# Kernel tuning notes

Hardware: AMD Instinct MI355X
Metric: run time of the kernel (lower is better)

The kernel has to match this reference:

```python
import jax, jax.numpy as jnp
import numpy as np

# ---- static config (matches init_kwargs) ----
DIM = 96
H = W = D = 28
WS = 7            # window size
SS = 3            # shift size
NH = 4            # num heads
HD = DIM // NH    # head dim
SCALE = HD ** -0.5
NWIN_TOK = WS ** 3  # 343 tokens per window
HIDDEN = int(DIM * 4.0)
RPB_SIZE = (2 * WS - 1) ** 3


def _relative_position_index(ws):
    # faithful to source: rel[...,0] *= 2*ws-1 ; rel[...,1] *= 2*ws-1
    coords = np.stack(np.meshgrid(np.arange(ws), np.arange(ws), np.arange(ws), indexing='ij'))
    flat = coords.reshape(3, -1)                      # (3, N)
    rel = flat[:, :, None] - flat[:, None, :]         # (3, N, N)
    rel = rel.transpose(1, 2, 0).astype(np.int64)     # (N, N, 3)
    rel += ws - 1
    rel[:, :, 0] *= 2 * ws - 1
    rel[:, :, 1] *= 2 * ws - 1
    return rel.sum(-1)                                # (N, N)


def _attn_mask(Hh, Ww, Dd, ws, ss):
    img = np.zeros((1, Hh, Ww, Dd, 1), np.float32)
    cnt = 0
    sl = (slice(0, -ws), slice(-ws, -ss), slice(-ss, None))
    for a in sl:
        for b in sl:
            for c in sl:
                img[:, a, b, c, :] = cnt
                cnt += 1
    x = img.reshape(1, Hh // ws, ws, Ww // ws, ws, Dd // ws, ws, 1)
    mw = x.transpose(0, 1, 3, 5, 2, 4, 6, 7).reshape(-1, ws ** 3)  # (nW, N)
    am = mw[:, None, :] - mw[:, :, None]                           # (nW, N, N)
    return np.where(am != 0, -100.0, 0.0).astype(np.float32)


RPI = jnp.asarray(_relative_position_index(WS))          # (N, N) int
ATTN_MASK = jnp.asarray(_attn_mask(H, W, D, WS, SS))     # (nW, N, N)


def _ln(x, w, b, eps=1e-5):
    mu = x.mean(-1, keepdims=True)
    xc = x - mu
    var = (xc * xc).mean(-1, keepdims=True)
    return xc * jax.lax.rsqrt(var + eps) * w + b


def _window_partition(x):
    # x: (B, H, W, D, C) -> (B*nW, N, C)
    B, _, _, _, C = x.shape
    x = x.reshape(B, H // WS, WS, W // WS, WS, D // WS, WS, C)
    return x.transpose(0, 1, 3, 5, 2, 4, 6, 7).reshape(-1, NWIN_TOK, C)


def _window_reverse(wins, B):
    C = wins.shape[-1]
    x = wins.reshape(B, H // WS, W // WS, D // WS, WS, WS, WS, C)
    return x.transpose(0, 1, 4, 2, 5, 3, 6, 7).reshape(B, H, W, D, C)


def setup_inputs() -> dict:
    key = jax.random.key(0)
    ks = jax.random.split(key, 16)
    p = lambda k, shape, s: (jax.random.normal(k, shape, jnp.float32) * s)
    return {
        'x': jax.random.normal(ks[0], (4, H * W * D, DIM), jnp.float32),
        'norm1_w': jnp.ones((DIM,), jnp.float32),
        'norm1_b': jnp.zeros((DIM,), jnp.float32),
        'qkv_w': p(ks[1], (DIM, 3 * DIM), 0.02),   # (in, out)
        'qkv_b': jnp.zeros((3 * DIM,), jnp.float32),
        'rpb_table': p(ks[2], (RPB_SIZE, NH), 0.02),
        'proj_w': p(ks[3], (DIM, DIM), 0.02),
        'proj_b': jnp.zeros((DIM,), jnp.float32),
        'norm2_w': jnp.ones((DIM,), jnp.float32),
        'norm2_b': jnp.zeros((DIM,), jnp.float32),
        'fc1_w': p(ks[4], (DIM, HIDDEN), 0.02),
        'fc1_b': jnp.zeros((HIDDEN,), jnp.float32),
        'fc2_w': p(ks[5], (HIDDEN, DIM), 0.02),
        'fc2_b': jnp.zeros((DIM,), jnp.float32),
    }


def reference(x, norm1_w, norm1_b, qkv_w, qkv_b, rpb_table, proj_w, proj_b,
              norm2_w, norm2_b, fc1_w, fc1_b, fc2_w, fc2_b):
    B, L, C = x.shape
    shortcut = x

    xn = _ln(x, norm1_w, norm1_b).reshape(B, H, W, D, C)
    # cyclic shift (SW-MSA)
    xs = jnp.roll(xn, (-SS, -SS, -SS), axis=(1, 2, 3))
    xw = _window_partition(xs)                        # (B_, N, C)
    B_ = xw.shape[0]
    Nn = NWIN_TOK

    qkv = (xw @ qkv_w + qkv_b).reshape(B_, Nn, 3, NH, HD).transpose(2, 0, 3, 1, 4)
    q, k, v = qkv[0], qkv[1], qkv[2]                  # (B_, h, N, hd)
    attn = jnp.einsum('bhnd,bhmd->bhnm', q * SCALE, k)

    # relative position bias gather: (N*N,) -> (N, N, h) -> (h, N, N)
    rpb = rpb_table[RPI.reshape(-1)].reshape(Nn, Nn, NH).transpose(2, 0, 1)
    attn = attn + rpb[None]

    nW = ATTN_MASK.shape[0]
    attn = attn.reshape(B, nW, NH, Nn, Nn) + ATTN_MASK[None, :, None]
    attn = jax.nn.softmax(attn.reshape(B_, NH, Nn, Nn), axis=-1)

    out = jnp.einsum('bhnm,bhmd->bhnd', attn, v).transpose(0, 2, 1, 3).reshape(B_, Nn, C)
    out = out @ proj_w + proj_b

    xr = _window_reverse(out, B)
    xr = jnp.roll(xr, (SS, SS, SS), axis=(1, 2, 3)).reshape(B, L, C)

    x = shortcut + xr                                  # drop_path = 0 (eval)
    y = _ln(x, norm2_w, norm2_b)
    y = jax.nn.gelu(y @ fc1_w + fc1_b, approximate=False)
    return x + (y @ fc2_w + fc2_b)
```

## Files before the change

### kernel.cpp

```cpp
#include <hip/hip_runtime.h>

#define NTOK 343
#define NP   352
#define SCALE 0.2041241452319315f
#define VSTR 360
#define PSTR 40

typedef __attribute__((ext_vector_type(8))) short bf16x8;
typedef __attribute__((ext_vector_type(4))) float f32x4;

__device__ __forceinline__ unsigned short f2bf(float f){
  unsigned u = __builtin_bit_cast(unsigned, f);
  u += 0x7fffu + ((u >> 16) & 1u);
  return (unsigned short)(u >> 16);
}
__device__ __forceinline__ float bfel(const uint4& q, int t){
  unsigned u = (&q.x)[t >> 1];
  u = (t & 1) ? (u & 0xffff0000u) : (u << 16);
  return __builtin_bit_cast(float, u);
}
__device__ __forceinline__ unsigned pk2(float a, float b){
  unsigned ua = __builtin_bit_cast(unsigned, a) + 0x8000u;
  unsigned ub = __builtin_bit_cast(unsigned, b) + 0x8000u;
  return __builtin_amdgcn_perm(ub, ua, 0x07060302u);
}
__device__ __forceinline__ unsigned pkrn(float a, float b){
  return (unsigned)f2bf(a) | ((unsigned)f2bf(b) << 16);
}
__device__ __forceinline__ int region(int g){ return (g < 21) ? 0 : ((g < 25) ? 1 : 2); }

__global__ __launch_bounds__(256) void k_rpb(const float* __restrict__ tab, float* __restrict__ rpbB){
  const int bid = blockIdx.x, tid = threadIdx.x;
  const int lane = tid >> 2, reg = tid & 3;
  const int qt = bid % 22, tmp = bid / 22, kt = tmp % 22, hh = tmp / 22;
  const int n = lane & 15, qd = lane >> 4;
  const int i = qt * 16 + n;
  const int j = kt * 16 + qd * 4 + reg;
  float v;
  if (j >= NTOK) v = -1e30f;
  else if (i >= NTOK) v = 0.f;
  else {
    int r1 = i / 49, rm = i - r1 * 49, r2 = rm / 7, r3 = rm - r2 * 7;
    int j1 = j / 49, jm = j - j1 * 49, j2 = jm / 7, j3 = jm - j2 * 7;
    int idx = 13 * ((r1 - j1) + (r2 - j2) + 12) + (r3 - j3) + 6;
    v = tab[idx * 4 + hh];
  }
  rpbB[(size_t)bid * 256 + tid] = v;
}

__global__ __launch_bounds__(256) void k_wprep1(const float* __restrict__ qw, unsigned short* __restrict__ wQ){
  int p = blockIdx.x * 256 + threadIdx.x;
  int e = p & 7, m = (p >> 3) & 15, cell = p >> 7;
  int mt = cell / 12, kq = cell - mt * 12;
  wQ[p] = f2bf(qw[(kq * 8 + e) * 288 + mt * 16 + m]);
}

__global__ __launch_bounds__(256) void k_wprep2(
    const float* __restrict__ pw, const float* __restrict__ w1g, const float* __restrict__ w2g,
    unsigned short* __restrict__ w1F, unsigned short* __restrict__ w2F, unsigned short* __restrict__ wP)
{
  int p = blockIdx.x * 256 + threadIdx.x;
  if (p < 36864){
    int e = p & 7, m = (p >> 3) & 15, cell = p >> 7;
    int mt = cell / 12, q = cell - mt * 12;
    w1F[p] = f2bf(w1g[(q * 8 + e) * 384 + mt * 16 + m]);
  } else if (p < 73728){
    int p2 = p - 36864;
    int e = p2 & 7, m = (p2 >> 3) & 15, cell = p2 >> 7;
    int omt = cell / 48, q = cell - omt * 48;
    w2F[p2] = f2bf(w2g[(q * 8 + e) * 96 + omt * 16 + m]);
  } else {
    int p3 = p - 73728;
    int e = p3 & 7, m = (p3 >> 3) & 15, cell = p3 >> 7;
    int mt = cell / 12, kq = cell - mt * 12;
    wP[p3] = f2bf(pw[(kq * 8 + e) * 96 + mt * 16 + m]);
  }
}

__global__ __launch_bounds__(256, 4) void k_qkv(
    const float* __restrict__ x, const float* __restrict__ n1w, const float* __restrict__ n1b,
    const unsigned short* __restrict__ wQ, const float* __restrict__ qb,
    unsigned short* __restrict__ qS, unsigned short* __restrict__ kS, unsigned short* __restrict__ vS)
{
  __shared__ __align__(16) unsigned short xnF[11 * 12 * 16 * 8];
  const int blk = blockIdx.x, w = blk >> 1, half = blk & 1;
  const int b = w >> 6, wl = w & 63;
  const int wx = wl >> 4, wy = (wl >> 2) & 3, wz = wl & 3;
  const int tid = threadIdx.x, lane = tid & 63, wv = tid >> 6;

  const float g1 = n1w[lane], h1 = n1b[lane];
  const float g2 = (lane < 32) ? n1w[64 + lane] : 0.f;
  const float h2 = (lane < 32) ? n1b[64 + lane] : 0.f;
  for (int r = wv; r < 176; r += 4){
    int tl = half * 176 + r;
    int tok = (tl < NTOK) ? tl : NTOK - 1;
    int tx = tok / 49, rm = tok - tx * 49, ty = rm / 7, tz = rm - ty * 7;
    int sx = (wx * 7 + tx + 3) % 28, sy = (wy * 7 + ty + 3) % 28, sz = (wz * 7 + tz + 3) % 28;
    const float* xr = x + ((size_t)b * 21952 + ((sx * 28 + sy) * 28 + sz)) * 96;
    float v1 = xr[lane];
    float v2 = (lane < 32) ? xr[64 + lane] : 0.f;
    float s = v1 + v2, sq = v1 * v1 + v2 * v2;
    #pragma unroll
    for (int off = 32; off; off >>= 1){ s += __shfl_xor(s, off); sq += __shfl_xor(sq, off); }
    float mu = s * (1.f / 96.f);
    float rs = rsqrtf(sq * (1.f / 96.f) - mu * mu + 1e-5f);
    int nt = r >> 4, n = r & 15;
    xnF[((nt * 12 + (lane >> 3)) * 16 + n) * 8 + (lane & 7)] = f2bf((v1 - mu) * rs * g1 + h1);
    if (lane < 32){
      int cc = 64 + lane;
      xnF[((nt * 12 + (cc >> 3)) * 16 + n) * 8 + (cc & 7)] = f2bf((v2 - mu) * rs * g2 + h2);
    }
  }
  __syncthreads();

  const int ln = lane & 15, qd = lane >> 4;
  bf16x8 bfr[3][3];
  int nts[3], toks[3];
  #pragma unroll
  for (int t = 0; t < 3; t++){
    int nt = wv + 4 * t;
    nts[t] = (nt < 11) ? nt : -1;
    int ntc = (nt < 11) ? nt : 0;
    toks[t] = half * 176 + ntc * 16 + ln;
    #pragma unroll
    for (int ks = 0; ks < 3; ks++)
      bfr[t][ks] = *(const bf16x8*)(xnF + ((ntc * 12 + ks * 4 + qd) * 16 + ln) * 8);
  }
  for (int mt = 0; mt < 18; mt++){
    bf16x8 afr[3];
    #pragma unroll
    for (int ks = 0; ks < 3; ks++)
      afr[ks] = *(const bf16x8*)(wQ + ((mt * 12 + ks * 4 + qd) * 16 + ln) * 8);
    f32x4 acc[3];
    #pragma unroll
    for (int t = 0; t < 3; t++){ acc[t][0] = 0.f; acc[t][1] = 0.f; acc[t][2] = 0.f; acc[t][3] = 0.f; }
    #pragma unroll
    for (int ks = 0; ks < 3; ks++)
      #pragma unroll
      for (int t = 0; t < 3; t++)
        acc[t] = __builtin_amdgcn_mfma_f32_16x16x32_bf16(afr[ks], bfr[t][ks], acc[t], 0, 0, 0);
    const int o0 = mt * 16 + 4 * qd;
    float4 bv = *(const float4*)(qb + o0);
    const int s3 = o0 / 96, om = o0 - s3 * 96, hh = om / 24, d = om - hh * 24;
    const float sc = (s3 == 0) ? SCALE : 1.f;
    unsigned short* base = (s3 == 0) ? qS : ((s3 == 1) ? kS : vS);
    unsigned short* hb = base + ((size_t)(w * 4 + hh)) * 8232 + d;
    #pragma unroll
    for (int t = 0; t < 3; t++){
      if (nts[t] < 0) continue;
      if (toks[t] < NTOK){
        uint2 st;
        st.x = pkrn((acc[t][0] + bv.x) * sc, (acc[t][1] + bv.y) * sc);
        st.y = pkrn((acc[t][2] + bv.z) * sc, (acc[t][3] + bv.w) * sc);
        *(uint2*)(hb + (size_t)toks[t] * 24) = st;
      }
    }
  }
}

__global__ __launch_bounds__(256, 2) void k_attn(
    const unsigned short* __restrict__ qS, const unsigned short* __restrict__ kS,
    const unsigned short* __restrict__ vS, const float* __restrict__ rpbB,
    unsigned short* __restrict__ aO)
{
  __shared__ __align__(16) unsigned short Ksh[NP * 24];
  __shared__ __align__(16) unsigned short VTsh[24 * VSTR];
  __shared__ __align__(16) unsigned short Psh[4 * 16 * PSTR];
  __shared__ __align__(8) unsigned char lab8[NP];

  const int blk = blockIdx.x, w = blk >> 2, h = blk & 3;
  const int tid = threadIdx.x, lane = tid & 63, wv = tid >> 6;
  const int ln = lane & 15, qd = lane >> 4;

  {
    const unsigned* kg = (const unsigned*)(kS + (size_t)blk * 8232);
    unsigned* kd = (unsigned*)Ksh;
    for (int i = tid; i < 4224; i += 256) kd[i] = (i < 4116) ? kg[i] : 0u;
    const unsigned* vg = (const unsigned*)(vS + (size_t)blk * 8232);
    for (int i = tid; i < 4116; i += 256){
      unsigned v = vg[i];
      int e0 = 2 * i, key = e0 / 24, d = e0 - key * 24;
      VTsh[d * VSTR + key] = (unsigned short)(v & 0xffffu);
      VTsh[(d + 1) * VSTR + key] = (unsigned short)(v >> 16);
    }
    for (int i = tid; i < 24 * 13; i += 256){
      int d = i / 13, kk = 343 + (i - d * 13);
      VTsh[d * VSTR + kk] = 0;
    }
    const int wl = w & 63, wx = wl >> 4, wy = (wl >> 2) & 3, wz = wl & 3;
    for (int n = tid; n < NP; n += 256){
      int tx = n / 49, nm = n - tx * 49, ty = nm / 7, tz = nm - ty * 7;
      lab8[n] = (n < NTOK) ? (unsigned char)(region(wx*7+tx)*9 + region(wy*7+ty)*3 + region(wz*7+tz)) : (unsigned char)0;
    }
  }
  __syncthreads();

  bf16x8 qf[6];
  int labQ[6], qts[6];
  #pragma unroll
  for (int t = 0; t < 6; t++){
    int qtr = wv + 4 * t;
    bool val = qtr < 22;
    qts[t] = val ? qtr : -1;
    int qt = val ? qtr : 0;
    int query = qt * 16 + ln;
    uint4 qv = *(const uint4*)(qS + (size_t)blk * 8232 + (size_t)query * 24 + qd * 8);
    if (qd == 3){ qv.x = 0; qv.y = 0; qv.z = 0; qv.w = 0; }
    qf[t] = __builtin_bit_cast(bf16x8, qv);
    labQ[t] = lab8[qt * 16 + ln];
  }

  f32x4 accO[6][2];
  float ssum[6];
  #pragma unroll
  for (int t = 0; t < 6; t++){
    ssum[t] = 0.f;
    #pragma unroll
    for (int d2 = 0; d2 < 2; d2++){ accO[t][d2][0]=0.f; accO[t][d2][1]=0.f; accO[t][d2][2]=0.f; accO[t][d2][3]=0.f; }
  }
  const float* biasBase = rpbB + (size_t)h * (22 * 22 * 256);
  unsigned short* pb = Psh + wv * 16 * PSTR + ln * PSTR;
  const unsigned short* pr = Psh + wv * 16 * PSTR + ln * PSTR + qd * 8;
  const int vt1row = 16 + (ln & 7);
  const f32x4 zf = {0.f, 0.f, 0.f, 0.f};

  for (int kp = 0; kp < 11; kp++){
    uint4 kv0 = *(const uint4*)(Ksh + (kp * 32 + ln) * 24 + qd * 8);
    uint4 kv1 = *(const uint4*)(Ksh + (kp * 32 + 16 + ln) * 24 + qd * 8);
    bf16x8 kf0 = __builtin_bit_cast(bf16x8, kv0);
    bf16x8 kf1 = __builtin_bit_cast(bf16x8, kv1);
    bf16x8 vf0 = *(const bf16x8*)(VTsh + ln * VSTR + kp * 32 + qd * 8);
    bf16x8 vf1 = *(const bf16x8*)(VTsh + vt1row * VSTR + kp * 32 + qd * 8);
    const unsigned* l32 = (const unsigned*)lab8;
    unsigned la = l32[kp * 8 + qd];
    unsigned lb = l32[kp * 8 + 4 + qd];
    int kl0[4], kl1[4];
    #pragma unroll
    for (int r = 0; r < 4; r++){ kl0[r] = (la >> (8 * r)) & 255; kl1[r] = (lb >> (8 * r)) & 255; }

    #pragma unroll
    for (int t = 0; t < 6; t++){
      if (qts[t] < 0) continue;
      const int qt = qts[t];
      f32x4 s0 = __builtin_amdgcn_mfma_f32_16x16x32_bf16(kf0, qf[t], zf, 0, 0, 0);
      f32x4 s1 = __builtin_amdgcn_mfma_f32_16x16x32_bf16(kf1, qf[t], zf, 0, 0, 0);
      const float* bp = biasBase + (((size_t)(2 * kp) * 22 + qt) * 64 + lane) * 4;
      float4 b0 = *(const float4*)bp;
      float4 b1 = *(const float4*)(bp + 22 * 256);
      const int lq = labQ[t];
      float e0[4], e1[4];
      #pragma unroll
      for (int r = 0; r < 4; r++){
        float ev = __expf(s0[r] + (&b0.x)[r]);
        e0[r] = (kl0[r] == lq) ? ev : 0.f;
      }
      #pragma unroll
      for (int r = 0; r < 4; r++){
        float ev = __expf(s1[r] + (&b1.x)[r]);
        e1[r] = (kl1[r] == lq) ? ev : 0.f;
      }
      ssum[t] += ((e0[0] + e0[1]) + (e0[2] + e0[3])) + ((e1[0] + e1[1]) + (e1[2] + e1[3]));
      uint2 w0; w0.x = pk2(e0[0], e0[1]); w0.y = pk2(e0[2], e0[3]);
      uint2 w1; w1.x = pk2(e1[0], e1[1]); w1.y = pk2(e1[2], e1[3]);
      *(uint2*)(pb + 4 * qd)      = w0;
      *(uint2*)(pb + 16 + 4 * qd) = w1;
      bf16x8 pf = *(const bf16x8*)pr;
      accO[t][0] = __builtin_amdgcn_mfma_f32_16x16x32_bf16(vf0, pf, accO[t][0], 0, 0, 0);
      accO[t][1] = __builtin_amdgcn_mfma_f32_16x16x32_bf16(vf1, pf, accO[t][1], 0, 0, 0);
    }
  }

  #pragma unroll
  for (int t = 0; t < 6; t++){
    if (qts[t] < 0) continue;
    float s = ssum[t];
    s += __shfl_xor(s, 16);
    s += __shfl_xor(s, 32);
    float inv = 1.f / s;
    int query = qts[t] * 16 + ln;
    if (query < NTOK){
      unsigned short* dst = aO + (size_t)w * 32928 + (size_t)query * 96 + h * 24;
      uint2 o0;
      o0.x = pkrn(accO[t][0][0] * inv, accO[t][0][1] * inv);
      o0.y = pkrn(accO[t][0][2] * inv, accO[t][0][3] * inv);
      *(uint2*)(dst + 4 * qd) = o0;
      if (qd < 2){
        uint2 o1;
        o1.x = pkrn(accO[t][1][0] * inv, accO[t][1][1] * inv);
        o1.y = pkrn(accO[t][1][2] * inv, accO[t][1][3] * inv);
        *(uint2*)(dst + 16 + 4 * qd) = o1;
      }
    }
  }
}

__global__ __launch_bounds__(256, 4) void k_proj(
    const unsigned short* __restrict__ aO, const unsigned short* __restrict__ wP,
    const float* __restrict__ pb, const float* __restrict__ x, float* __restrict__ out)
{
  __shared__ __align__(16) unsigned short aF[11 * 12 * 16 * 8];
  const int blk = blockIdx.x, w = blk >> 1, half = blk & 1;
  const int b = w >> 6, wl = w & 63;
  const int wx = wl >> 4, wy = (wl >> 2) & 3, wz = wl & 3;
  const int tid = threadIdx.x, lane = tid & 63, wv = tid >> 6;

  for (int i = tid; i < 2112; i += 256){
    int r = i / 12, kq = i - r * 12;
    int tl = half * 176 + r;
    uint4 v;
    if (tl < NTOK) v = *(const uint4*)(aO + (size_t)w * 32928 + (size_t)tl * 96 + kq * 8);
    else { v.x = 0u; v.y = 0u; v.z = 0u; v.w = 0u; }
    int nt = r >> 4, n = r & 15;
    *(uint4*)(aF + ((nt * 12 + kq) * 16 + n) * 8) = v;
  }
  __syncthreads();

  const int ln = lane & 15, qd = lane >> 4;
  bf16x8 bfr[3][3];
  int nts[3]; size_t oi[3]; bool tv[3];
  #pragma unroll
  for (int t = 0; t < 3; t++){
    int nt = wv + 4 * t;
    nts[t] = (nt < 11) ? nt : -1;
    int ntc = (nt < 11) ? nt : 0;
    int tok = half * 176 + ntc * 16 + ln;
    tv[t] = (nts[t] >= 0) && (tok < NTOK);
    int tk = (tok < NTOK) ? tok : 0;
    int tx = tk / 49, rm = tk - tx * 49, ty = rm / 7, tz = rm - ty * 7;
    int sx = (wx * 7 + tx + 3) % 28, sy = (wy * 7 + ty + 3) % 28, sz = (wz * 7 + tz + 3) % 28;
    oi[t] = ((size_t)b * 21952 + ((sx * 28 + sy) * 28 + sz)) * 96;
    #pragma unroll
    for (int ks = 0; ks < 3; ks++)
      bfr[t][ks] = *(const bf16x8*)(aF + ((ntc * 12 + ks * 4 + qd) * 16 + ln) * 8);
  }
  for (int mt = 0; mt < 6; mt++){
    bf16x8 afr[3];
    #pragma unroll
    for (int ks = 0; ks < 3; ks++)
      afr[ks] = *(const bf16x8*)(wP + ((mt * 12 + ks * 4 + qd) * 16 + ln) * 8);
    f32x4 acc[3];
    #pragma unroll
    for (int t = 0; t < 3; t++){ acc[t][0] = 0.f; acc[t][1] = 0.f; acc[t][2] = 0.f; acc[t][3] = 0.f; }
    #pragma unroll
    for (int ks = 0; ks < 3; ks++)
      #pragma unroll
      for (int t = 0; t < 3; t++)
        acc[t] = __builtin_amdgcn_mfma_f32_16x16x32_bf16(afr[ks], bfr[t][ks], acc[t], 0, 0, 0);
    const int c0 = mt * 16 + 4 * qd;
    float4 bv = *(const float4*)(pb + c0);
    #pragma unroll
    for (int t = 0; t < 3; t++){
      if (!tv[t]) continue;
      float4 cur = *(const float4*)(x + oi[t] + c0);
      float4 o;
      o.x = acc[t][0] + bv.x + cur.x;
      o.y = acc[t][1] + bv.y + cur.y;
      o.z = acc[t][2] + bv.z + cur.z;
      o.w = acc[t][3] + bv.w + cur.w;
      *(float4*)(out + oi[t] + c0) = o;
    }
  }
}

__global__ __launch_bounds__(256, 4) void k_mlp(
    float* __restrict__ io, const float* __restrict__ n2w, const float* __restrict__ n2b,
    const unsigned short* __restrict__ w1F, const float* __restrict__ b1g,
    const unsigned short* __restrict__ w2F, const float* __restrict__ b2g)
{
  __shared__ __align__(16) unsigned short xnF[2 * 12 * 16 * 8];
  __shared__ __align__(16) unsigned short hF[2 * 48 * 16 * 8];
  const int tid = threadIdx.x, lane = tid & 63, wv = tid >> 6;
  const size_t row0 = (size_t)blockIdx.x * 32;

  const float g1 = n2w[lane], c1 = n2b[lane];
  const float g2 = (lane < 32) ? n2w[64 + lane] : 0.f;
  const float c2 = (lane < 32) ? n2b[64 + lane] : 0.f;
  for (int r = wv; r < 32; r += 4){
    const float* xr = io + (row0 + r) * 96;
    float v1 = xr[lane], v2 = (lane < 32) ? xr[64 + lane] : 0.f;
    float s = v1 + v2, sq = v1 * v1 + v2 * v2;
    #pragma unroll
    for (int off = 32; off; off >>= 1){ s += __shfl_xor(s, off); sq += __shfl_xor(sq, off); }
    float mu = s * (1.f / 96.f);
    float rs = rsqrtf(sq * (1.f / 96.f) - mu * mu + 1e-5f);
    int nt = r >> 4, n = r & 15;
    xnF[((nt * 12 + (lane >> 3)) * 16 + n) * 8 + (lane & 7)] = f2bf((v1 - mu) * rs * g1 + c1);
    if (lane < 32){
      int cc = 64 + lane;
      xnF[((nt * 12 + (cc >> 3)) * 16 + n) * 8 + (cc & 7)] = f2bf((v2 - mu) * rs * g2 + c2);
    }
  }
  __syncthreads();

  const int h = lane & 15, q = lane >> 4;
  const int nt = wv & 1, mh = wv >> 1;

  f32x4 acc[12];
  #pragma unroll
  for (int mt = 0; mt < 12; mt++){
    int o0 = (mh * 12 + mt) * 16 + 4 * q;
    float4 bv = *(const float4*)(b1g + o0);
    acc[mt][0] = bv.x; acc[mt][1] = bv.y; acc[mt][2] = bv.z; acc[mt][3] = bv.w;
  }
  for (int ks = 0; ks < 3; ks++){
    bf16x8 bfr = *(const bf16x8*)(xnF + ((nt * 12 + ks * 4 + q) * 16 + h) * 8);
    #pragma unroll
    for (int mt = 0; mt < 12; mt++){
      bf16x8 afr = *(const bf16x8*)(w1F + (((mh * 12 + mt) * 12 + ks * 4 + q) * 16 + h) * 8);
      acc[mt] = __builtin_amdgcn_mfma_f32_16x16x32_bf16(afr, bfr, acc[mt], 0, 0, 0);
    }
  }
  #pragma unroll
  for (int mt = 0; mt < 12; mt++){
    int o0 = (mh * 12 + mt) * 16 + 4 * q;
    unsigned short pk[4];
    #pragma unroll
    for (int rg = 0; rg < 4; rg++){
      float v = acc[mt][rg];
      pk[rg] = f2bf(0.5f * v * (1.f + erff(v * 0.70710678118654752f)));
    }
    unsigned short* d = hF + ((nt * 48 + (o0 >> 3)) * 16 + h) * 8 + (o0 & 7);
    uint2 pkv; pkv.x = (unsigned)pk[0] | ((unsigned)pk[1] << 16);
    pkv.y = (unsigned)pk[2] | ((unsigned)pk[3] << 16);
    *(uint2*)d = pkv;
  }
  __syncthreads();

  f32x4 acc2[3];
  #pragma unroll
  for (int mt = 0; mt < 3; mt++){
    int o0 = (mh * 3 + mt) * 16 + 4 * q;
    float4 bv = *(const float4*)(b2g + o0);
    acc2[mt][0] = bv.x; acc2[mt][1] = bv.y; acc2[mt][2] = bv.z; acc2[mt][3] = bv.w;
  }
  for (int ks = 0; ks < 12; ks++){
    bf16x8 bfr = *(const bf16x8*)(hF + ((nt * 48 + ks * 4 + q) * 16 + h) * 8);
    #pragma unroll
    for (int mt = 0; mt < 3; mt++){
      bf16x8 afr = *(const bf16x8*)(w2F + (((mh * 3 + mt) * 48 + ks * 4 + q) * 16 + h) * 8);
      acc2[mt] = __builtin_amdgcn_mfma_f32_16x16x32_bf16(afr, bfr, acc2[mt], 0, 0, 0);
    }
  }
  float* orow = io + (row0 + nt * 16 + h) * 96;
  #pragma unroll
  for (int mt = 0; mt < 3; mt++){
    int o0 = (mh * 3 + mt) * 16 + 4 * q;
    float4 cur = *(const float4*)(orow + o0);
    cur.x += acc2[mt][0]; cur.y += acc2[mt][1]; cur.z += acc2[mt][2]; cur.w += acc2[mt][3];
    *(float4*)(orow + o0) = cur;
  }
}

extern "C" void kernel_launch(void* const* d_in, const int* in_sizes, int n_in,
                              void* d_out, int out_size, void* d_ws, size_t ws_size,
                              hipStream_t stream)
{
  const float* x      = (const float*)d_in[0];
  const float* n1w    = (const float*)d_in[1];
  const float* n1b    = (const float*)d_in[2];
  const float* qkvw   = (const float*)d_in[3];
  const float* qkvb   = (const float*)d_in[4];
  const float* rpbtab = (const float*)d_in[5];
  const float* projw  = (const float*)d_in[6];
  const float* projb  = (const float*)d_in[7];
  const float* n2w    = (const float*)d_in[8];
  const float* n2b    = (const float*)d_in[9];
  const float* fc1w   = (const float*)d_in[10];
  const float* fc1b   = (const float*)d_in[11];
  const float* fc2w   = (const float*)d_in[12];
  const float* fc2b   = (const float*)d_in[13];
  float* out = (float*)d_out;

  unsigned short* qS = (unsigned short*)d_ws;
  unsigned short* kS = qS + 8429568;
  unsigned short* vS = kS + 8429568;
  unsigned short* aO = vS + 8429568;
  float* rpbB = (float*)(aO + 8429568);
  unsigned short* wQ  = aO;
  unsigned short* w1F = qS;
  unsigned short* w2F = qS + 36864;
  unsigned short* wP  = qS + 73728;

  k_rpb   <<<dim3(1936), dim3(256), 0, stream>>>(rpbtab, rpbB);
  k_wprep1<<<dim3(108),  dim3(256), 0, stream>>>(qkvw, wQ);
  k_qkv   <<<dim3(512),  dim3(256), 0, stream>>>(x, n1w, n1b, wQ, qkvb, qS, kS, vS);
  k_attn  <<<dim3(1024), dim3(256), 0, stream>>>(qS, kS, vS, rpbB, aO);
  k_wprep2<<<dim3(324),  dim3(256), 0, stream>>>(projw, fc1w, fc2w, w1F, w2F, wP);
  k_proj  <<<dim3(512),  dim3(256), 0, stream>>>(aO, wP, projb, x, out);
  k_mlp   <<<dim3(2744), dim3(256), 0, stream>>>(out, n2w, n2b, w1F, fc1b, w2F, fc2b);
}
```

Baseline: 318.9 us.

## Restructure window attention: bf16 bias in MFMA accumulator, exp2, pre-transposed V, ones-row rowsum

The relative-position bias is stored as bf16 pre-scaled by log2(e) and loaded as the MFMA accumulator init, and Q is scaled by log2(e), so softmax uses exp2 with no separate bias add. k_qkv now writes V already transposed, which removes the shared-memory transpose in k_attn. K is read straight from global memory instead of staged in LDS. An extra all-ones row in V^T makes the PV MFMA produce the softmax row sum, dropping the scalar sum. Less LDS lets launch bounds rise to 4 blocks per SM, but bias precision drops to bf16 and the transposed V stores in k_qkv are scattered 2-byte writes.

Result: faster. 285.2 us (-10.6%).

```diff
diff --git a/kernel.cpp b/kernel.cpp
--- a/kernel.cpp
+++ b/kernel.cpp
@@ -3,6 +3,7 @@
 #define NTOK 343
 #define NP   352
 #define SCALE 0.2041241452319315f
+#define LOG2E 1.44269504088896340736f
 #define VSTR 360
 #define PSTR 40
 
@@ -14,11 +15,8 @@
   u += 0x7fffu + ((u >> 16) & 1u);
   return (unsigned short)(u >> 16);
 }
-__device__ __forceinline__ float bfel(const uint4& q, int t){
-  unsigned u = (&q.x)[t >> 1];
-  u = (t & 1) ? (u & 0xffff0000u) : (u << 16);
-  return __builtin_bit_cast(float, u);
-}
+__device__ __forceinline__ float bflo(unsigned u){ return __builtin_bit_cast(float, u << 16); }
+__device__ __forceinline__ float bfhi(unsigned u){ return __builtin_bit_cast(float, u & 0xffff0000u); }
 __device__ __forceinline__ unsigned pk2(float a, float b){
   unsigned ua = __builtin_bit_cast(unsigned, a) + 0x8000u;
   unsigned ub = __builtin_bit_cast(unsigned, b) + 0x8000u;
@@ -29,23 +27,26 @@
 }
 __device__ __forceinline__ int region(int g){ return (g < 21) ? 0 : ((g < 25) ? 1 : 2); }
 
-__global__ __launch_bounds__(256) void k_rpb(const float* __restrict__ tab, float* __restrict__ rpbB){
-  const int bid = blockIdx.x, tid = threadIdx.x;
-  const int lane = tid >> 2, reg = tid & 3;
-  const int qt = bid % 22, tmp = bid / 22, kt = tmp % 22, hh = tmp / 22;
-  const int n = lane & 15, qd = lane >> 4;
-  const int i = qt * 16 + n;
-  const int j = kt * 16 + qd * 4 + reg;
-  float v;
-  if (j >= NTOK) v = -1e30f;
-  else if (i >= NTOK) v = 0.f;
-  else {
-    int r1 = i / 49, rm = i - r1 * 49, r2 = rm / 7, r3 = rm - r2 * 7;
-    int j1 = j / 49, jm = j - j1 * 49, j2 = jm / 7, j3 = jm - j2 * 7;
-    int idx = 13 * ((r1 - j1) + (r2 - j2) + 12) + (r3 - j3) + 6;
-    v = tab[idx * 4 + hh];
-  }
-  rpbB[(size_t)bid * 256 + tid] = v;
+__global__ __launch_bounds__(256) void k_rpb(const float* __restrict__ tab, unsigned short* __restrict__ rpbH){
+  const int bid = blockIdx.x;
+  const int qt = bid % 22, t2 = bid / 22, kp = t2 % 11, h = t2 / 11;
+  for (int e = threadIdx.x; e < 512; e += 256){
+    int lane = e >> 3, slot = e & 7;
+    int kth = slot >> 2, reg = slot & 3;
+    int n = lane & 15, qd = lane >> 4;
+    int i = qt * 16 + n;
+    int j = (2 * kp + kth) * 16 + qd * 4 + reg;
+    float v;
+    if (j >= NTOK) v = -1e30f;
+    else if (i >= NTOK) v = 0.f;
+    else {
+      int r1 = i / 49, rm = i - r1 * 49, r2 = rm / 7, r3 = rm - r2 * 7;
+      int j1 = j / 49, jm = j - j1 * 49, j2 = jm / 7, j3 = jm - j2 * 7;
+      int idx = 13 * ((r1 - j1) + (r2 - j2) + 12) + (r3 - j3) + 6;
+      v = tab[idx * 4 + h] * LOG2E;
+    }
+    rpbH[(size_t)bid * 512 + e] = f2bf(v);
+  }
 }
 
 __global__ __launch_bounds__(256) void k_wprep1(const float* __restrict__ qw, unsigned short* __restrict__ wQ){
@@ -80,7 +81,7 @@
 __global__ __launch_bounds__(256, 4) void k_qkv(
     const float* __restrict__ x, const float* __restrict__ n1w, const float* __restrict__ n1b,
     const unsigned short* __restrict__ wQ, const float* __restrict__ qb,
-    unsigned short* __restrict__ qS, unsigned short* __restrict__ kS, unsigned short* __restrict__ vS)
+    unsigned short* __restrict__ qS, unsigned short* __restrict__ kS, unsigned short* __restrict__ vT)
 {
   __shared__ __align__(16) unsigned short xnF[11 * 12 * 16 * 8];
   const int blk = blockIdx.x, w = blk >> 1, half = blk & 1;
@@ -141,30 +142,38 @@
         acc[t] = __builtin_amdgcn_mfma_f32_16x16x32_bf16(afr[ks], bfr[t][ks], acc[t], 0, 0, 0);
     const int o0 = mt * 16 + 4 * qd;
     float4 bv = *(const float4*)(qb + o0);
-    const int s3 = o0 / 96, om = o0 - s3 * 96, hh = om / 24, d = om - hh * 24;
-    const float sc = (s3 == 0) ? SCALE : 1.f;
-    unsigned short* base = (s3 == 0) ? qS : ((s3 == 1) ? kS : vS);
-    unsigned short* hb = base + ((size_t)(w * 4 + hh)) * 8232 + d;
-    #pragma unroll
-    for (int t = 0; t < 3; t++){
-      if (nts[t] < 0) continue;
-      if (toks[t] < NTOK){
+    const int s3 = o0 / 96, om = o0 - s3 * 96, hh = om / 24, dd = om - hh * 24;
+    if (s3 < 2){
+      const float sc = (s3 == 0) ? (SCALE * LOG2E) : 1.f;
+      unsigned short* hb = ((s3 == 0) ? qS : kS) + ((size_t)(w * 4 + hh)) * 8232 + dd;
+      #pragma unroll
+      for (int t = 0; t < 3; t++){
+        if (nts[t] < 0 || toks[t] >= NTOK) continue;
         uint2 st;
         st.x = pkrn((acc[t][0] + bv.x) * sc, (acc[t][1] + bv.y) * sc);
         st.y = pkrn((acc[t][2] + bv.z) * sc, (acc[t][3] + bv.w) * sc);
         *(uint2*)(hb + (size_t)toks[t] * 24) = st;
       }
-    }
-  }
-}
-
-__global__ __launch_bounds__(256, 2) void k_attn(
+    } else {
+      unsigned short* hb = vT + ((size_t)(w * 4 + hh)) * 8256 + (size_t)dd * 344;
+      #pragma unroll
+      for (int t = 0; t < 3; t++){
+        if (nts[t] < 0 || toks[t] >= NTOK) continue;
+        hb[0 * 344 + toks[t]] = f2bf(acc[t][0] + bv.x);
+        hb[1 * 344 + toks[t]] = f2bf(acc[t][1] + bv.y);
+        hb[2 * 344 + toks[t]] = f2bf(acc[t][2] + bv.z);
+        hb[3 * 344 + toks[t]] = f2bf(acc[t][3] + bv.w);
+      }
+    }
+  }
+}
+
+__global__ __launch_bounds__(256, 4) void k_attn(
     const unsigned short* __restrict__ qS, const unsigned short* __restrict__ kS,
-    const unsigned short* __restrict__ vS, const float* __restrict__ rpbB,
+    const unsigned short* __restrict__ vT, const unsigned short* __restrict__ rpbH,
     unsigned short* __restrict__ aO)
 {
-  __shared__ __align__(16) unsigned short Ksh[NP * 24];
-  __shared__ __align__(16) unsigned short VTsh[24 * VSTR];
+  __shared__ __align__(16) unsigned short VTsh[25 * VSTR];
   __shared__ __align__(16) unsigned short Psh[4 * 16 * PSTR];
   __shared__ __align__(8) unsigned char lab8[NP];
 
@@ -173,20 +182,17 @@
   const int ln = lane & 15, qd = lane >> 4;
 
   {
-    const unsigned* kg = (const unsigned*)(kS + (size_t)blk * 8232);
-    unsigned* kd = (unsigned*)Ksh;
-    for (int i = tid; i < 4224; i += 256) kd[i] = (i < 4116) ? kg[i] : 0u;
-    const unsigned* vg = (const unsigned*)(vS + (size_t)blk * 8232);
-    for (int i = tid; i < 4116; i += 256){
-      unsigned v = vg[i];
-      int e0 = 2 * i, key = e0 / 24, d = e0 - key * 24;
-      VTsh[d * VSTR + key] = (unsigned short)(v & 0xffffu);
-      VTsh[(d + 1) * VSTR + key] = (unsigned short)(v >> 16);
-    }
-    for (int i = tid; i < 24 * 13; i += 256){
-      int d = i / 13, kk = 343 + (i - d * 13);
-      VTsh[d * VSTR + kk] = 0;
-    }
+    const unsigned* vg = (const unsigned*)(vT + (size_t)blk * 8256);
+    unsigned* vd = (unsigned*)VTsh;
+    for (int i = tid; i < 4128; i += 256){
+      int d = i / 172, c = i - d * 172;
+      vd[d * 180 + c] = vg[i];
+    }
+    for (int i = tid; i < 192; i += 256){
+      int d = i >> 3, c = i & 7;
+      vd[d * 180 + 172 + c] = 0u;
+    }
+    for (int i = tid; i < 180; i += 256) vd[24 * 180 + i] = 0x3f803f80u;
     const int wl = w & 63, wx = wl >> 4, wy = (wl >> 2) & 3, wz = wl & 3;
     for (int n = tid; n < NP; n += 256){
       int tx = n / 49, nm = n - tx * 49, ty = nm / 7, tz = nm - ty * 7;
@@ -211,26 +217,24 @@
   }
 
   f32x4 accO[6][2];
-  float ssum[6];
-  #pragma unroll
-  for (int t = 0; t < 6; t++){
-    ssum[t] = 0.f;
+  #pragma unroll
+  for (int t = 0; t < 6; t++)
     #pragma unroll
     for (int d2 = 0; d2 < 2; d2++){ accO[t][d2][0]=0.f; accO[t][d2][1]=0.f; accO[t][d2][2]=0.f; accO[t][d2][3]=0.f; }
-  }
-  const float* biasBase = rpbB + (size_t)h * (22 * 22 * 256);
+
+  const unsigned short* biasBase = rpbH + (size_t)h * (11 * 22 * 512);
   unsigned short* pb = Psh + wv * 16 * PSTR + ln * PSTR;
   const unsigned short* pr = Psh + wv * 16 * PSTR + ln * PSTR + qd * 8;
-  const int vt1row = 16 + (ln & 7);
-  const f32x4 zf = {0.f, 0.f, 0.f, 0.f};
+  const int vrow1 = (ln < 8) ? (16 + ln) : 24;
+  const size_t kbase = (size_t)blk * 8232;
 
   for (int kp = 0; kp < 11; kp++){
-    uint4 kv0 = *(const uint4*)(Ksh + (kp * 32 + ln) * 24 + qd * 8);
-    uint4 kv1 = *(const uint4*)(Ksh + (kp * 32 + 16 + ln) * 24 + qd * 8);
+    uint4 kv0 = *(const uint4*)(kS + kbase + (size_t)(kp * 32 + ln) * 24 + qd * 8);
+    uint4 kv1 = *(const uint4*)(kS + kbase + (size_t)(kp * 32 + 16 + ln) * 24 + qd * 8);
     bf16x8 kf0 = __builtin_bit_cast(bf16x8, kv0);
     bf16x8 kf1 = __builtin_bit_cast(bf16x8, kv1);
     bf16x8 vf0 = *(const bf16x8*)(VTsh + ln * VSTR + kp * 32 + qd * 8);
-    bf16x8 vf1 = *(const bf16x8*)(VTsh + vt1row * VSTR + kp * 32 + qd * 8);
+    bf16x8 vf1 = *(const bf16x8*)(VTsh + vrow1 * VSTR + kp * 32 + qd * 8);
     const unsigned* l32 = (const unsigned*)lab8;
     unsigned la = l32[kp * 8 + qd];
     unsigned lb = l32[kp * 8 + 4 + qd];
@@ -242,24 +246,24 @@
     for (int t = 0; t < 6; t++){
       if (qts[t] < 0) continue;
       const int qt = qts[t];
-      f32x4 s0 = __builtin_amdgcn_mfma_f32_16x16x32_bf16(kf0, qf[t], zf, 0, 0, 0);
-      f32x4 s1 = __builtin_amdgcn_mfma_f32_16x16x32_bf16(kf1, qf[t], zf, 0, 0, 0);
-      const float* bp = biasBase + (((size_t)(2 * kp) * 22 + qt) * 64 + lane) * 4;
-      float4 b0 = *(const float4*)bp;
-      float4 b1 = *(const float4*)(bp + 22 * 256);
+      uint4 bv = *(const uint4*)(biasBase + (((size_t)kp * 22 + qt) * 64 + lane) * 8);
+      f32x4 C0, C1;
+      C0[0] = bflo(bv.x); C0[1] = bfhi(bv.x); C0[2] = bflo(bv.y); C0[3] = bfhi(bv.y);
+      C1[0] = bflo(bv.z); C1[1] = bfhi(bv.z); C1[2] = bflo(bv.w); C1[3] = bfhi(bv.w);
+      f32x4 s0 = __builtin_amdgcn_mfma_f32_16x16x32_bf16(kf0, qf[t], C0, 0, 0, 0);
+      f32x4 s1 = __builtin_amdgcn_mfma_f32_16x16x32_bf16(kf1, qf[t], C1, 0, 0, 0);
       const int lq = labQ[t];
       float e0[4], e1[4];
       #pragma unroll
       for (int r = 0; r < 4; r++){
-        float ev = __expf(s0[r] + (&b0.x)[r]);
+        float ev = __builtin_amdgcn_exp2f(s0[r]);
         e0[r] = (kl0[r] == lq) ? ev : 0.f;
       }
       #pragma unroll
       for (int r = 0; r < 4; r++){
-        float ev = __expf(s1[r] + (&b1.x)[r]);
+        float ev = __builtin_amdgcn_exp2f(s1[r]);
         e1[r] = (kl1[r] == lq) ? ev : 0.f;
       }
-      ssum[t] += ((e0[0] + e0[1]) + (e0[2] + e0[3])) + ((e1[0] + e1[1]) + (e1[2] + e1[3]));
       uint2 w0; w0.x = pk2(e0[0], e0[1]); w0.y = pk2(e0[2], e0[3]);
       uint2 w1; w1.x = pk2(e1[0], e1[1]); w1.y = pk2(e1[2], e1[3]);
       *(uint2*)(pb + 4 * qd)      = w0;
@@ -273,10 +277,8 @@
   #pragma unroll
   for (int t = 0; t < 6; t++){
     if (qts[t] < 0) continue;
-    float s = ssum[t];
-    s += __shfl_xor(s, 16);
-    s += __shfl_xor(s, 32);
-    float inv = 1.f / s;
+    float ss = __shfl(accO[t][1][0], 32 + ln);
+    float inv = 1.f / ss;
     int query = qts[t] * 16 + ln;
     if (query < NTOK){
       unsigned short* dst = aO + (size_t)w * 32928 + (size_t)query * 96 + h * 24;
@@ -471,20 +473,20 @@
   const float* fc2b   = (const float*)d_in[13];
   float* out = (float*)d_out;
 
-  unsigned short* qS = (unsigned short*)d_ws;
-  unsigned short* kS = qS + 8429568;
-  unsigned short* vS = kS + 8429568;
-  unsigned short* aO = vS + 8429568;
-  float* rpbB = (float*)(aO + 8429568);
+  unsigned short* qS   = (unsigned short*)d_ws;
+  unsigned short* kS   = qS + 8429568;
+  unsigned short* vT   = kS + 8429568;
+  unsigned short* aO   = vT + 8454144;
+  unsigned short* rpbH = aO + 8429568;
   unsigned short* wQ  = aO;
   unsigned short* w1F = qS;
   unsigned short* w2F = qS + 36864;
   unsigned short* wP  = qS + 73728;
 
-  k_rpb   <<<dim3(1936), dim3(256), 0, stream>>>(rpbtab, rpbB);
+  k_rpb   <<<dim3(968),  dim3(256), 0, stream>>>(rpbtab, rpbH);
   k_wprep1<<<dim3(108),  dim3(256), 0, stream>>>(qkvw, wQ);
-  k_qkv   <<<dim3(512),  dim3(256), 0, stream>>>(x, n1w, n1b, wQ, qkvb, qS, kS, vS);
-  k_attn  <<<dim3(1024), dim3(256), 0, stream>>>(qS, kS, vS, rpbB, aO);
+  k_qkv   <<<dim3(512),  dim3(256), 0, stream>>>(x, n1w, n1b, wQ, qkvb, qS, kS, vT);
+  k_attn  <<<dim3(1024), dim3(256), 0, stream>>>(qS, kS, vT, rpbH, aO);
   k_wprep2<<<dim3(324),  dim3(256), 0, stream>>>(projw, fc1w, fc2w, w1F, w2F, wP);
   k_proj  <<<dim3(512),  dim3(256), 0, stream>>>(aO, wP, projb, x, out);
   k_mlp   <<<dim3(2744), dim3(256), 0, stream>>>(out, n2w, n2b, w1F, fc1b, w2F, fc2b);
```
